# Kernel optimization log

Hardware: AMD Instinct MI355X
Metric: run time of the kernel (lower is better)

Reference implementation:

```python
import jax, jax.numpy as jnp
import numpy as np

N_NODES = 100000
N_EDGES = 1600000
IN_FEATS = 128
NUM_HEADS = 4
OUT_FEATS = 32
NEG_SLOPE = 0.2


def setup_inputs() -> dict:
    key = jax.random.key(0)
    k1, k2, k3, k4, k5, k6 = jax.random.split(key, 6)
    feat = jax.random.normal(k1, (N_NODES, IN_FEATS), dtype=jnp.float32)
    src = jax.random.randint(k2, (N_EDGES,), 0, N_NODES, dtype=jnp.int32)
    dst = jnp.sort(jax.random.randint(k3, (N_EDGES,), 0, N_NODES, dtype=jnp.int32))
    # glorot-style scale ~ VarianceScaling(sqrt(2), fan_avg)
    w_scale = np.sqrt(2.0 * 2.0 / (IN_FEATS + NUM_HEADS * OUT_FEATS)).astype(np.float32)
    a_scale = np.sqrt(2.0 * 2.0 / (1 + OUT_FEATS)).astype(np.float32)
    W = jax.random.normal(k4, (IN_FEATS, NUM_HEADS * OUT_FEATS), dtype=jnp.float32) * w_scale
    attn_l = jax.random.normal(k5, (NUM_HEADS, OUT_FEATS), dtype=jnp.float32) * a_scale
    attn_r = jax.random.normal(k6, (NUM_HEADS, OUT_FEATS), dtype=jnp.float32) * a_scale
    return {"feat": feat, "src": src, "dst": dst, "W": W, "attn_l": attn_l, "attn_r": attn_r}


def reference(feat, src, dst, W, attn_l, attn_r):
    # Linear projection: [N, H, D]
    ft = (feat @ W).reshape(-1, NUM_HEADS, OUT_FEATS)
    # Per-node attention halves: [N, H]
    el = jnp.einsum("nhd,hd->nh", ft, attn_l)
    er = jnp.einsum("nhd,hd->nh", ft, attn_r)
    # Edge scores: e_ij = LeakyReLU(el[src] + er[dst])  -> [E, H]
    e = el[src] + er[dst]
    e = jnp.where(e > 0, e, NEG_SLOPE * e)
    # edge_softmax: per-destination segment softmax over incoming edges
    emax = jax.ops.segment_max(e, dst, num_segments=N_NODES)  # [N, H]
    ex = jnp.exp(e - emax[dst])                               # [E, H]
    esum = jax.ops.segment_sum(ex, dst, num_segments=N_NODES)  # [N, H]
    a = ex / esum[dst]                                         # [E, H]
    # Weighted scatter-sum aggregation: sum_j a_ij * W h_j -> [N, H, D]
    m = ft[src] * a[:, :, None]
    out = jax.ops.segment_sum(m, dst, num_segments=N_NODES)
    return out
```

## Files before the change

kernel.cpp:

```cpp
#include <hip/hip_runtime.h>

#define N_NODES 100000
#define N_EDGES 1600000
#define NUM_HEADS 4
#define NEG_SLOPE 0.2f
#define LDSTRIDE 136
#define SEG_BLOCKS 1563

typedef __attribute__((ext_vector_type(8))) short bf16x8;
typedef __attribute__((ext_vector_type(4))) float f32x4;

__device__ __forceinline__ unsigned short f2bf(float x) {
    union { float f; unsigned u; } v; v.f = x;
    unsigned r = v.u + 0x7fffu + ((v.u >> 16) & 1u);
    return (unsigned short)(r >> 16);
}
__device__ __forceinline__ float bflo(unsigned v) { return __uint_as_float(v << 16); }
__device__ __forceinline__ float bfhi(unsigned v) { return __uint_as_float(v & 0xffff0000u); }

__global__ __launch_bounds__(256) void prep_seg_kernel(
    const int* __restrict__ dst, int* __restrict__ seg,
    const float* __restrict__ W, const float* __restrict__ attn_l,
    const float* __restrict__ attn_r, unsigned short* __restrict__ Wt2)
{
    const int b = blockIdx.x;
    if (b < SEG_BLOCKS) {
        int i4 = b * 256 + threadIdx.x;
        if (i4 >= N_EDGES / 4) return;
        const int e0 = 4 * i4;
        const int4 d = ((const int4*)dst)[i4];
        const int dp = (e0 == 0) ? -1 : dst[e0 - 1];
        for (int n = dp + 1; n <= d.x; ++n) seg[n] = e0;
        for (int n = d.x + 1; n <= d.y; ++n) seg[n] = e0 + 1;
        for (int n = d.y + 1; n <= d.z; ++n) seg[n] = e0 + 2;
        for (int n = d.z + 1; n <= d.w; ++n) seg[n] = e0 + 3;
        if (e0 + 4 == N_EDGES)
            for (int n = d.w + 1; n <= N_NODES; ++n) seg[n] = N_EDGES;
    } else {
        int idx = (b - SEG_BLOCKS) * 256 + threadIdx.x;
        if (idx >= 136 * 128) return;
        int n = idx >> 7, k = idx & 127;
        if (n < 128) {
            Wt2[idx] = f2bf(W[k * 128 + n]);
        } else {
            int h = (n - 128) & 3;
            const float* av = ((n - 128) < 4 ? attn_l : attn_r) + h * 32;
            const float* col = W + k * 128 + h * 32;
            float s = 0.f;
#pragma unroll
            for (int d2 = 0; d2 < 32; ++d2) s += col[d2] * av[d2];
            Wt2[idx] = f2bf(s);
        }
    }
}

__global__ __launch_bounds__(256) void gemm_kernel(
    const float* __restrict__ feat, const unsigned short* __restrict__ Wt2,
    unsigned short* __restrict__ ft, float* __restrict__ el,
    float* __restrict__ er)
{
    __shared__ __align__(16) unsigned short B_lds[136 * LDSTRIDE];
    __shared__ __align__(16) unsigned short A_lds[64 * LDSTRIDE];
    const int t = threadIdx.x;
    const int nbase = blockIdx.x * 64;

    {
        const int4* Wt4 = (const int4*)Wt2;
#pragma unroll
        for (int i = 0; i < 9; ++i) {
            int idx = t + 256 * i;
            if (idx < 2176) {
                int n = idx >> 4, cg = idx & 15;
                *(int4*)(&B_lds[n * LDSTRIDE + cg * 8]) = Wt4[idx];
            }
        }
    }
    {
        const float4* f4 = (const float4*)feat;
#pragma unroll
        for (int i = 0; i < 8; ++i) {
            int idx = t + 256 * i;
            int node = idx >> 5, kg = idx & 31;
            int g = nbase + node; if (g >= N_NODES) g = N_NODES - 1;
            float4 f = f4[g * 32 + kg];
            ushort4 u;
            u.x = f2bf(f.x); u.y = f2bf(f.y); u.z = f2bf(f.z); u.w = f2bf(f.w);
            *(ushort4*)(&A_lds[node * LDSTRIDE + kg * 4]) = u;
        }
    }
    __syncthreads();

    const int w = t >> 6, lane = t & 63;
    const int l15 = lane & 15, quad = lane >> 4;

    f32x4 acc[9];
#pragma unroll
    for (int c = 0; c < 9; ++c) acc[c] = (f32x4){0.f, 0.f, 0.f, 0.f};

    const unsigned short* Arow = &A_lds[(w * 16 + l15) * LDSTRIDE + quad * 8];
    const unsigned short* Brow = &B_lds[l15 * LDSTRIDE + quad * 8];
    const unsigned short* Brow8 = &B_lds[(128 + (l15 & 7)) * LDSTRIDE + quad * 8];
#pragma unroll
    for (int ks = 0; ks < 4; ++ks) {
        bf16x8 a = *(const bf16x8*)(Arow + ks * 32);
#pragma unroll
        for (int c = 0; c < 8; ++c) {
            bf16x8 b = *(const bf16x8*)(Brow + (c * 16) * LDSTRIDE + ks * 32);
            acc[c] = __builtin_amdgcn_mfma_f32_16x16x32_bf16(a, b, acc[c], 0, 0, 0);
        }
        bf16x8 b8 = *(const bf16x8*)(Brow8 + ks * 32);
        acc[8] = __builtin_amdgcn_mfma_f32_16x16x32_bf16(a, b8, acc[8], 0, 0, 0);
    }

#pragma unroll
    for (int reg = 0; reg < 4; ++reg) {
        const int g = nbase + w * 16 + quad * 4 + reg;
        if (g < N_NODES) {
            if (l15 < 4)      el[g * 4 + l15] = acc[8][reg];
            else if (l15 < 8) er[g * 4 + (l15 - 4)] = acc[8][reg];
        }
    }

#pragma unroll
    for (int c = 0; c < 8; ++c) {
#pragma unroll
        for (int reg = 0; reg < 4; ++reg) {
            A_lds[(w * 16 + quad * 4 + reg) * LDSTRIDE + c * 16 + l15] =
                f2bf(acc[c][reg]);
        }
    }
    __syncthreads();

#pragma unroll
    for (int i = 0; i < 4; ++i) {
        int idx = t + 256 * i;
        int node = idx >> 4, cg = idx & 15;
        int g = nbase + node;
        if (g < N_NODES) {
            int4 val = *(const int4*)(&A_lds[node * LDSTRIDE + cg * 8]);
            *(int4*)(&ft[(size_t)g * 128 + cg * 8]) = val;
        }
    }
}

__global__ __launch_bounds__(256) void aggregate_kernel(
    const unsigned short* __restrict__ ft, const float* __restrict__ el,
    const float* __restrict__ er, const int* __restrict__ src,
    const int* __restrict__ seg, float* __restrict__ out)
{
    const int node = blockIdx.x * 4 + (threadIdx.x >> 6);
    if (node >= N_NODES) return;
    const int lane = threadIdx.x & 63;
    const int h4 = lane & 3;
    const int q4 = lane >> 2;
    const int qt = lane >> 4;
    const int l15 = lane & 15;
    const int hf = l15 >> 2;

    const int beg = __builtin_amdgcn_readfirstlane(seg[node]);
    const int end = __builtin_amdgcn_readfirstlane(seg[node + 1]);
    const float er_h = er[node * 4 + h4];

    float dpart = 0.f;
    float4 accA = make_float4(0.f, 0.f, 0.f, 0.f);
    float4 accB = make_float4(0.f, 0.f, 0.f, 0.f);

    for (int c0 = beg; c0 < end; c0 += 16) {
        const int L = end - c0;
        int cidx = c0 + q4; if (cidx >= end) cidx = end - 1;
        const int s = src[cidx];
        float e = el[s * 4 + h4] + er_h;
        e = (e > 0.f) ? e : NEG_SLOPE * e;
        const float p = (q4 < L) ? __expf(e) : 0.f;
        dpart += p;

        int sj[4];
#pragma unroll
        for (int k = 0; k < 4; ++k) sj[k] = __shfl(s, 16 * k + 4 * qt);
        int4 v[4];
#pragma unroll
        for (int k = 0; k < 4; ++k)
            v[k] = *(const int4*)(ft + (((size_t)(unsigned)sj[k]) << 7) + l15 * 8);
#pragma unroll
        for (int k = 0; k < 4; ++k) {
            const float pj = __shfl(p, 16 * k + 4 * qt + hf);
            accA.x += pj * bflo(v[k].x); accA.y += pj * bfhi(v[k].x);
            accA.z += pj * bflo(v[k].y); accA.w += pj * bfhi(v[k].y);
            accB.x += pj * bflo(v[k].z); accB.y += pj * bfhi(v[k].z);
            accB.z += pj * bflo(v[k].w); accB.w += pj * bfhi(v[k].w);
        }
    }

    dpart += __shfl_xor(dpart, 4);
    dpart += __shfl_xor(dpart, 8);
    dpart += __shfl_xor(dpart, 16);
    dpart += __shfl_xor(dpart, 32);
    accA.x += __shfl_xor(accA.x, 16); accA.y += __shfl_xor(accA.y, 16);
    accA.z += __shfl_xor(accA.z, 16); accA.w += __shfl_xor(accA.w, 16);
    accB.x += __shfl_xor(accB.x, 16); accB.y += __shfl_xor(accB.y, 16);
    accB.z += __shfl_xor(accB.z, 16); accB.w += __shfl_xor(accB.w, 16);
    accA.x += __shfl_xor(accA.x, 32); accA.y += __shfl_xor(accA.y, 32);
    accA.z += __shfl_xor(accA.z, 32); accA.w += __shfl_xor(accA.w, 32);
    accB.x += __shfl_xor(accB.x, 32); accB.y += __shfl_xor(accB.y, 32);
    accB.z += __shfl_xor(accB.z, 32); accB.w += __shfl_xor(accB.w, 32);

    const float dh = __shfl(dpart, hf);
    const float inv = (dh > 0.f) ? 1.f / dh : 0.f;

    if (qt == 0) {
        float4 o0 = make_float4(accA.x * inv, accA.y * inv, accA.z * inv, accA.w * inv);
        float4 o1 = make_float4(accB.x * inv, accB.y * inv, accB.z * inv, accB.w * inv);
        float* op = out + (size_t)node * 128 + l15 * 8;
        *(float4*)op = o0;
        *(float4*)(op + 4) = o1;
    }
}

extern "C" void kernel_launch(void* const* d_in, const int* in_sizes, int n_in,
                              void* d_out, int out_size, void* d_ws, size_t ws_size,
                              hipStream_t stream) {
    const float* feat   = (const float*)d_in[0];
    const int*   src    = (const int*)d_in[1];
    const int*   dst    = (const int*)d_in[2];
    const float* W      = (const float*)d_in[3];
    const float* attn_l = (const float*)d_in[4];
    const float* attn_r = (const float*)d_in[5];
    float* out = (float*)d_out;

    unsigned short* ft = (unsigned short*)d_ws;
    float* el  = (float*)(ft + (size_t)12800000);
    float* er  = el + 400000;
    unsigned short* Wt2 = (unsigned short*)(er + 400000);
    int* seg = (int*)(Wt2 + 136 * 128);

    prep_seg_kernel<<<SEG_BLOCKS + 68, 256, 0, stream>>>(
        dst, seg, W, attn_l, attn_r, Wt2);
    gemm_kernel<<<(N_NODES + 63) / 64, 256, 0, stream>>>(feat, Wt2, ft, el, er);
    aggregate_kernel<<<(N_NODES + 3) / 4, 256, 0, stream>>>(
        ft, el, er, src, seg, out);
}
```

Baseline: 191.2 us.

## Load GEMM A operand directly to registers and recompute edge weights per lane

The GEMM kernel drops the A staging buffer in LDS: each lane loads its feat row slice straight from global memory, converts it to bf16 in registers, and reuses the B buffer for the output transpose after an extra barrier. It also adds a min-blocks-per-CU launch bound, so the smaller LDS footprint can allow more blocks per CU. In the aggregation kernel each lane now loads the src indices and el values it needs and computes its own exponentials, which removes the shuffles for indices and weights and shortens the denominator reduction. In exchange the aggregation issues redundant src/el loads and exp work across lanes, and the GEMM A loads are less coalesced.

```diff
diff --git a/kernel.cpp b/kernel.cpp
--- a/kernel.cpp
+++ b/kernel.cpp
@@ -54,13 +54,12 @@
     }
 }
 
-__global__ __launch_bounds__(256) void gemm_kernel(
+__global__ __launch_bounds__(256, 4) void gemm_kernel(
     const float* __restrict__ feat, const unsigned short* __restrict__ Wt2,
     unsigned short* __restrict__ ft, float* __restrict__ el,
     float* __restrict__ er)
 {
     __shared__ __align__(16) unsigned short B_lds[136 * LDSTRIDE];
-    __shared__ __align__(16) unsigned short A_lds[64 * LDSTRIDE];
     const int t = threadIdx.x;
     const int nbase = blockIdx.x * 64;
 
@@ -75,34 +74,30 @@
             }
         }
     }
-    {
-        const float4* f4 = (const float4*)feat;
-#pragma unroll
-        for (int i = 0; i < 8; ++i) {
-            int idx = t + 256 * i;
-            int node = idx >> 5, kg = idx & 31;
-            int g = nbase + node; if (g >= N_NODES) g = N_NODES - 1;
-            float4 f = f4[g * 32 + kg];
-            ushort4 u;
-            u.x = f2bf(f.x); u.y = f2bf(f.y); u.z = f2bf(f.z); u.w = f2bf(f.w);
-            *(ushort4*)(&A_lds[node * LDSTRIDE + kg * 4]) = u;
-        }
-    }
     __syncthreads();
 
     const int w = t >> 6, lane = t & 63;
     const int l15 = lane & 15, quad = lane >> 4;
 
+    int g = nbase + w * 16 + l15;
+    if (g >= N_NODES) g = N_NODES - 1;
+    const float4* f4 = (const float4*)feat + (size_t)g * 32 + quad * 2;
+
     f32x4 acc[9];
 #pragma unroll
     for (int c = 0; c < 9; ++c) acc[c] = (f32x4){0.f, 0.f, 0.f, 0.f};
 
-    const unsigned short* Arow = &A_lds[(w * 16 + l15) * LDSTRIDE + quad * 8];
     const unsigned short* Brow = &B_lds[l15 * LDSTRIDE + quad * 8];
     const unsigned short* Brow8 = &B_lds[(128 + (l15 & 7)) * LDSTRIDE + quad * 8];
 #pragma unroll
     for (int ks = 0; ks < 4; ++ks) {
-        bf16x8 a = *(const bf16x8*)(Arow + ks * 32);
+        float4 fa = f4[ks * 8];
+        float4 fb = f4[ks * 8 + 1];
+        bf16x8 a;
+        a[0] = (short)f2bf(fa.x); a[1] = (short)f2bf(fa.y);
+        a[2] = (short)f2bf(fa.z); a[3] = (short)f2bf(fa.w);
+        a[4] = (short)f2bf(fb.x); a[5] = (short)f2bf(fb.y);
+        a[6] = (short)f2bf(fb.z); a[7] = (short)f2bf(fb.w);
 #pragma unroll
         for (int c = 0; c < 8; ++c) {
             bf16x8 b = *(const bf16x8*)(Brow + (c * 16) * LDSTRIDE + ks * 32);
@@ -114,18 +109,19 @@
 
 #pragma unroll
     for (int reg = 0; reg < 4; ++reg) {
-        const int g = nbase + w * 16 + quad * 4 + reg;
-        if (g < N_NODES) {
-            if (l15 < 4)      el[g * 4 + l15] = acc[8][reg];
-            else if (l15 < 8) er[g * 4 + (l15 - 4)] = acc[8][reg];
-        }
-    }
-
+        const int gg = nbase + w * 16 + quad * 4 + reg;
+        if (gg < N_NODES) {
+            if (l15 < 4)      el[gg * 4 + l15] = acc[8][reg];
+            else if (l15 < 8) er[gg * 4 + (l15 - 4)] = acc[8][reg];
+        }
+    }
+
+    __syncthreads();
 #pragma unroll
     for (int c = 0; c < 8; ++c) {
 #pragma unroll
         for (int reg = 0; reg < 4; ++reg) {
-            A_lds[(w * 16 + quad * 4 + reg) * LDSTRIDE + c * 16 + l15] =
+            B_lds[(w * 16 + quad * 4 + reg) * LDSTRIDE + c * 16 + l15] =
                 f2bf(acc[c][reg]);
         }
     }
@@ -135,10 +131,10 @@
     for (int i = 0; i < 4; ++i) {
         int idx = t + 256 * i;
         int node = idx >> 4, cg = idx & 15;
-        int g = nbase + node;
-        if (g < N_NODES) {
-            int4 val = *(const int4*)(&A_lds[node * LDSTRIDE + cg * 8]);
-            *(int4*)(&ft[(size_t)g * 128 + cg * 8]) = val;
+        int gg = nbase + node;
+        if (gg < N_NODES) {
+            int4 val = *(const int4*)(&B_lds[node * LDSTRIDE + cg * 8]);
+            *(int4*)(&ft[(size_t)gg * 128 + cg * 8]) = val;
         }
     }
 }
@@ -151,39 +147,44 @@
     const int node = blockIdx.x * 4 + (threadIdx.x >> 6);
     if (node >= N_NODES) return;
     const int lane = threadIdx.x & 63;
-    const int h4 = lane & 3;
-    const int q4 = lane >> 2;
     const int qt = lane >> 4;
     const int l15 = lane & 15;
     const int hf = l15 >> 2;
 
     const int beg = __builtin_amdgcn_readfirstlane(seg[node]);
     const int end = __builtin_amdgcn_readfirstlane(seg[node + 1]);
-    const float er_h = er[node * 4 + h4];
+    const float er_h = er[node * 4 + hf];
 
     float dpart = 0.f;
     float4 accA = make_float4(0.f, 0.f, 0.f, 0.f);
     float4 accB = make_float4(0.f, 0.f, 0.f, 0.f);
 
     for (int c0 = beg; c0 < end; c0 += 16) {
-        const int L = end - c0;
-        int cidx = c0 + q4; if (cidx >= end) cidx = end - 1;
-        const int s = src[cidx];
-        float e = el[s * 4 + h4] + er_h;
-        e = (e > 0.f) ? e : NEG_SLOPE * e;
-        const float p = (q4 < L) ? __expf(e) : 0.f;
-        dpart += p;
-
-        int sj[4];
-#pragma unroll
-        for (int k = 0; k < 4; ++k) sj[k] = __shfl(s, 16 * k + 4 * qt);
+        const int cb = c0 + 4 * qt;
+        int s4[4];
+#pragma unroll
+        for (int k = 0; k < 4; ++k) {
+            int ci = cb + k;
+            s4[k] = src[ci < end ? ci : end - 1];
+        }
+        float ev[4];
+#pragma unroll
+        for (int k = 0; k < 4; ++k) ev[k] = el[s4[k] * 4 + hf];
+        float p[4];
+#pragma unroll
+        for (int k = 0; k < 4; ++k) {
+            float e = ev[k] + er_h;
+            e = (e > 0.f) ? e : NEG_SLOPE * e;
+            p[k] = (cb + k < end) ? __expf(e) : 0.f;
+            dpart += p[k];
+        }
         int4 v[4];
 #pragma unroll
         for (int k = 0; k < 4; ++k)
-            v[k] = *(const int4*)(ft + (((size_t)(unsigned)sj[k]) << 7) + l15 * 8);
+            v[k] = *(const int4*)(ft + (((size_t)(unsigned)s4[k]) << 7) + l15 * 8);
 #pragma unroll
         for (int k = 0; k < 4; ++k) {
-            const float pj = __shfl(p, 16 * k + 4 * qt + hf);
+            const float pj = p[k];
             accA.x += pj * bflo(v[k].x); accA.y += pj * bfhi(v[k].x);
             accA.z += pj * bflo(v[k].y); accA.w += pj * bfhi(v[k].y);
             accB.x += pj * bflo(v[k].z); accB.y += pj * bfhi(v[k].z);
@@ -191,21 +192,18 @@
         }
     }
 
-    dpart += __shfl_xor(dpart, 4);
-    dpart += __shfl_xor(dpart, 8);
-    dpart += __shfl_xor(dpart, 16);
-    dpart += __shfl_xor(dpart, 32);
+    dpart  += __shfl_xor(dpart, 16);
     accA.x += __shfl_xor(accA.x, 16); accA.y += __shfl_xor(accA.y, 16);
     accA.z += __shfl_xor(accA.z, 16); accA.w += __shfl_xor(accA.w, 16);
     accB.x += __shfl_xor(accB.x, 16); accB.y += __shfl_xor(accB.y, 16);
     accB.z += __shfl_xor(accB.z, 16); accB.w += __shfl_xor(accB.w, 16);
+    dpart  += __shfl_xor(dpart, 32);
     accA.x += __shfl_xor(accA.x, 32); accA.y += __shfl_xor(accA.y, 32);
     accA.z += __shfl_xor(accA.z, 32); accA.w += __shfl_xor(accA.w, 32);
     accB.x += __shfl_xor(accB.x, 32); accB.y += __shfl_xor(accB.y, 32);
     accB.z += __shfl_xor(accB.z, 32); accB.w += __shfl_xor(accB.w, 32);
 
-    const float dh = __shfl(dpart, hf);
-    const float inv = (dh > 0.f) ? 1.f / dh : 0.f;
+    const float inv = (dpart > 0.f) ? 1.f / dpart : 0.f;
 
     if (qt == 0) {
         float4 o0 = make_float4(accA.x * inv, accA.y * inv, accA.z * inv, accA.w * inv);
```

Measured after the change: 189.2 us. No clear change (-1.0%).
